# Kernel optimization log

Measured on AMD Instinct MI355X. Metric: run time of the kernel, lower is better.

## Reference

```python
import jax, jax.numpy as jnp
import numpy as np

D = 7            # tree max depth (n_locations = 4**D = 16384)
M = 128          # memory_dim
N_KEYS = sum(4 ** i for i in range(1, D + 1))      # 21844
N_INTERNAL = N_KEYS // 4                           # 5461


def setup_inputs() -> dict:
    key = jax.random.key(0)
    ks = jax.random.split(key, 6)
    B, C = 4096, 64
    hidden = jax.random.normal(ks[0], (B, C), dtype=jnp.float32)
    Wq = jax.random.normal(ks[1], (M, C), dtype=jnp.float32) * 0.05
    bq = jnp.zeros((M,), dtype=jnp.float32)
    states = jax.random.normal(ks[2], (N_KEYS, M), dtype=jnp.float32)
    Wk = jax.random.normal(ks[3], (D, M, M), dtype=jnp.float32) * 0.05
    bk = jnp.zeros((D, M), dtype=jnp.float32)
    return {"hidden": hidden, "Wq": Wq, "bq": bq, "states": states, "Wk": Wk, "bk": bk}


def reference(hidden, Wq, bq, states, Wk, bk):
    B = hidden.shape[0]
    # hidden_to_query (pre-training path uses class_to_query): [B, M]
    query = hidden @ Wq.T + bq
    # make_keys: per-depth state_to_key linear + activation on batch-independent states
    keys = []
    cursor = 0
    for i in range(D):
        n = 4 ** (i + 1)
        keys.append(jax.nn.relu(states[cursor:cursor + n] @ Wk[i].T + bk[i]))
        cursor += n
    keys = jnp.concatenate(keys, axis=0)               # [N_KEYS, M]
    # compute_scores: bmm(keys, query^T) -> [B, N_INTERNAL, 4]
    scores = jnp.einsum('km,bm->bk', keys, query).reshape(B, N_INTERNAL, 4)
    # to_location_distribution (is_consistent, pre_training): cumulative log-softmax down the tree
    logp = jax.nn.log_softmax(scores, axis=-1)         # [B, N_INTERNAL, 4]
    dists = []
    cur = None
    cursor = 0
    for d in range(1, D + 1):
        n_parents = 4 ** (d - 1)
        layer = logp[:, cursor:cursor + n_parents, :].reshape(B, 4 ** d)
        cur = layer if cur is None else jnp.repeat(cur, 4, axis=-1) + layer
        dists.append(cur)                              # [B, 4**d]
        cursor += n_parents
    return tuple(dists)
```

## Files before the change

### kernel.cpp

```cpp
#include <hip/hip_runtime.h>
#include <hip/hip_bf16.h>
#include <math.h>

#define MDIM 128
#define CDIM 64
#define NTILES 1366

typedef __attribute__((ext_vector_type(8))) __bf16 bf16x8;
typedef __attribute__((ext_vector_type(4))) float f32x4;

__global__ __launch_bounds__(256) void k_cvtw(const float* __restrict__ Wk,
                                              __hip_bfloat16* __restrict__ wkb) {
  const int i = blockIdx.x * 256 + threadIdx.x;
  float4 v = *reinterpret_cast<const float4*>(Wk + (size_t)i * 4);
  __hip_bfloat16 h[4];
  h[0] = __float2bfloat16(v.x); h[1] = __float2bfloat16(v.y);
  h[2] = __float2bfloat16(v.z); h[3] = __float2bfloat16(v.w);
  unsigned long long bits;
  __builtin_memcpy(&bits, h, 8);
  *reinterpret_cast<unsigned long long*>(wkb + (size_t)i * 4) = bits;
}

#define STR 144

__global__ __launch_bounds__(64) void k_keys_mfma(const float* __restrict__ states,
                                                  const __hip_bfloat16* __restrict__ wkb,
                                                  const float* __restrict__ bk,
                                                  bf16x8* __restrict__ keysF) {
  __shared__ __align__(16) __hip_bfloat16 sT[16 * STR];
  const int lane = threadIdx.x;
  const int c = lane & 15, hi = lane >> 4;
  int blk = blockIdx.x, d, t;
  if      (blk < 2)   { d = blk; t = 0; }
  else if (blk < 6)   { d = 2; t = blk - 2; }
  else if (blk < 22)  { d = 3; t = blk - 6; }
  else if (blk < 86)  { d = 4; t = blk - 22; }
  else if (blk < 342) { d = 5; t = blk - 86; }
  else                { d = 6; t = blk - 342; }
  const int cumArr[7] = {0, 4, 20, 84, 340, 1364, 5460};
  const int k0 = cumArr[d] + 16 * t;

  bf16x8 sb[4];
  const float* srow = states + (size_t)(k0 + c) * MDIM;
#pragma unroll
  for (int kf = 0; kf < 4; ++kf) {
    float4 a = *reinterpret_cast<const float4*>(srow + kf * 32 + hi * 8);
    float4 b = *reinterpret_cast<const float4*>(srow + kf * 32 + hi * 8 + 4);
    bf16x8 v;
    v[0] = (__bf16)a.x; v[1] = (__bf16)a.y; v[2] = (__bf16)a.z; v[3] = (__bf16)a.w;
    v[4] = (__bf16)b.x; v[5] = (__bf16)b.y; v[6] = (__bf16)b.z; v[7] = (__bf16)b.w;
    sb[kf] = v;
  }

  const __hip_bfloat16* wkd = wkb + (size_t)d * MDIM * MDIM;
  const float* bkd = bk + d * MDIM;

#pragma unroll
  for (int ct = 0; ct < 8; ++ct) {
    bf16x8 aw[4];
    const __hip_bfloat16* wrow = wkd + (size_t)(ct * 16 + c) * MDIM;
#pragma unroll
    for (int kf = 0; kf < 4; ++kf)
      aw[kf] = *reinterpret_cast<const bf16x8*>(wrow + kf * 32 + hi * 8);
    f32x4 acc = {};
#pragma unroll
    for (int kf = 0; kf < 4; ++kf)
      acc = __builtin_amdgcn_mfma_f32_16x16x32_bf16(aw[kf], sb[kf], acc, 0, 0, 0);
    float4 bias = *reinterpret_cast<const float4*>(bkd + ct * 16 + hi * 4);
    __hip_bfloat16 hv[4];
    hv[0] = __float2bfloat16(fmaxf(acc[0] + bias.x, 0.f));
    hv[1] = __float2bfloat16(fmaxf(acc[1] + bias.y, 0.f));
    hv[2] = __float2bfloat16(fmaxf(acc[2] + bias.z, 0.f));
    hv[3] = __float2bfloat16(fmaxf(acc[3] + bias.w, 0.f));
    unsigned long long bits;
    __builtin_memcpy(&bits, hv, 8);
    *reinterpret_cast<unsigned long long*>(&sT[c * STR + ct * 16 + 4 * hi]) = bits;
  }

#pragma unroll
  for (int kf = 0; kf < 4; ++kf) {
    bf16x8 v = *reinterpret_cast<const bf16x8*>(&sT[c * STR + kf * 32 + hi * 8]);
    keysF[(size_t)(blk * 4 + kf) * 64 + lane] = v;
  }
}

__global__ __launch_bounds__(128) void k_query(const float* __restrict__ hidden,
                                               const float* __restrict__ Wq,
                                               const float* __restrict__ bq,
                                               __hip_bfloat16* __restrict__ query) {
  __shared__ __align__(16) float sH[4][CDIM];
  const int b0 = blockIdx.x * 4;
  const int m  = threadIdx.x;
  for (int idx = m; idx < 4 * CDIM; idx += 128)
    sH[idx >> 6][idx & 63] = hidden[(size_t)b0 * CDIM + idx];
  __syncthreads();
  const float4* wrow = (const float4*)(Wq + (size_t)m * CDIM);
  float acc0 = 0.f, acc1 = 0.f, acc2 = 0.f, acc3 = 0.f;
#pragma unroll
  for (int kq = 0; kq < CDIM / 4; ++kq) {
    float4 w = wrow[kq];
    float4 a = *(const float4*)&sH[0][kq * 4];
    float4 b = *(const float4*)&sH[1][kq * 4];
    float4 c = *(const float4*)&sH[2][kq * 4];
    float4 e = *(const float4*)&sH[3][kq * 4];
    acc0 += w.x * a.x + w.y * a.y + w.z * a.z + w.w * a.w;
    acc1 += w.x * b.x + w.y * b.y + w.z * b.z + w.w * b.w;
    acc2 += w.x * c.x + w.y * c.y + w.z * c.z + w.w * c.w;
    acc3 += w.x * e.x + w.y * e.y + w.z * e.z + w.w * e.w;
  }
  const float bias = bq[m];
  query[(size_t)(b0 + 0) * MDIM + m] = __float2bfloat16(acc0 + bias);
  query[(size_t)(b0 + 1) * MDIM + m] = __float2bfloat16(acc1 + bias);
  query[(size_t)(b0 + 2) * MDIM + m] = __float2bfloat16(acc2 + bias);
  query[(size_t)(b0 + 3) * MDIM + m] = __float2bfloat16(acc3 + bias);
}

#define D7STR 68

struct Frag { bf16x8 f[4]; };

__device__ __forceinline__ void load_frags(const bf16x8* __restrict__ kF,
                                           int blk, Frag& fr, int lane) {
#pragma unroll
  for (int kf = 0; kf < 4; ++kf)
    fr.f[kf] = kF[(size_t)(blk * 4 + kf) * 64 + lane];
}

__device__ __forceinline__ float gather_par(const f32x4 cp, int u, int lane) {
  const int src = u * 16 + (lane & 15);
  const float g0 = __shfl(cp[0], src, 64);
  const float g1 = __shfl(cp[1], src, 64);
  const float g2 = __shfl(cp[2], src, 64);
  const float g3 = __shfl(cp[3], src, 64);
  const int hi = lane >> 4;
  const float p01 = (hi & 1) ? g1 : g0;
  const float p23 = (hi & 1) ? g3 : g2;
  return (hi & 2) ? p23 : p01;
}

__device__ __forceinline__ void tile_step(
    const bf16x8* __restrict__ kF, const Frag& cur, int nextBlk, Frag& nxt,
    const bf16x8 (&qf)[2][4], const f32x4* cumPrev, int u, f32x4 (&cumOut)[2],
    float* __restrict__ oPtr, size_t span, bool doStore, bool d1mask,
    float* __restrict__ ldsDst, int lane) {
  const int c = lane & 15, hi = lane >> 4;

  if (nextBlk >= 0) load_frags(kF, nextBlk, nxt, lane);

#pragma unroll
  for (int bt = 0; bt < 2; ++bt) {
    f32x4 acc = {};
    acc = __builtin_amdgcn_mfma_f32_16x16x32_bf16(cur.f[0], qf[bt][0], acc, 0, 0, 0);
    acc = __builtin_amdgcn_mfma_f32_16x16x32_bf16(cur.f[1], qf[bt][1], acc, 0, 0, 0);
    acc = __builtin_amdgcn_mfma_f32_16x16x32_bf16(cur.f[2], qf[bt][2], acc, 0, 0, 0);
    acc = __builtin_amdgcn_mfma_f32_16x16x32_bf16(cur.f[3], qf[bt][3], acc, 0, 0, 0);

    const float lse = __logf(__expf(acc[0]) + __expf(acc[1]) +
                             __expf(acc[2]) + __expf(acc[3]));
    float par = 0.f;
    if (cumPrev) par = gather_par(cumPrev[bt], u, lane);
    f32x4 cm;
    cm[0] = acc[0] - lse + par;
    cm[1] = acc[1] - lse + par;
    cm[2] = acc[2] - lse + par;
    cm[3] = acc[3] - lse + par;
    cumOut[bt] = cm;

    if (ldsDst) {
      *reinterpret_cast<f32x4*>(ldsDst + (bt * 16 + c) * D7STR) = cm;
    } else if (doStore && (!d1mask || hi == 0)) {
      float4 o;
      o.x = cm[0]; o.y = cm[1]; o.z = cm[2]; o.w = cm[3];
      *reinterpret_cast<float4*>(oPtr + (size_t)(bt * 16 + c) * span + hi * 4) = o;
    }
  }
}

__global__ __launch_bounds__(256) void k_tree(const bf16x8* __restrict__ kF,
                                              const __hip_bfloat16* __restrict__ query,
                                              float* __restrict__ out, int B) {
  __shared__ __align__(16) float sD7[4][32 * D7STR];
  __shared__ __align__(16) float sD6[4][32 * D7STR];

  const int tid  = threadIdx.x;
  const int lane = tid & 63;
  const int w    = tid >> 6;
  const int c    = lane & 15, hi = lane >> 4;

  const int S5  = blockIdx.x & 63;
  const int bg  = blockIdx.x >> 6;
  const int T4  = S5 >> 2;
  const int T3  = S5 >> 4;
  const int b0w = bg * 128 + w * 32;

  float* d7w = &sD7[w][0];
  float* d6w = &sD6[w][0];

  bf16x8 qf[2][4];
#pragma unroll
  for (int bt = 0; bt < 2; ++bt) {
    const __hip_bfloat16* qrow = query + (size_t)(b0w + bt * 16 + c) * MDIM;
#pragma unroll
    for (int kf = 0; kf < 4; ++kf)
      qf[bt][kf] = *reinterpret_cast<const bf16x8*>(qrow + kf * 32 + hi * 8);
  }

  Frag fA, fB;
  load_frags(kF, 0, fA, lane);

  f32x4 c1[2], c2[2], c3[2], c4[2], c5[2], c6[2], c7[2];

  tile_step(kF, fA, 1, fB, qf, nullptr, 0, c1,
            out + (size_t)b0w * 4, 4, S5 == 0, true, nullptr, lane);
  tile_step(kF, fB, 2 + T3, fA, qf, c1, 0, c2,
            out + (size_t)4 * B + (size_t)b0w * 16, 16, S5 == 0, false,
            nullptr, lane);
  tile_step(kF, fA, 6 + T4, fB, qf, c2, T3, c3,
            out + (size_t)20 * B + (size_t)b0w * 64 + 16 * T3, 64,
            (S5 & 15) == 0, false, nullptr, lane);
  tile_step(kF, fB, 22 + S5, fA, qf, c3, T4 & 3, c4,
            out + (size_t)84 * B + (size_t)b0w * 256 + 16 * T4, 256,
            (S5 & 3) == 0, false, nullptr, lane);
  tile_step(kF, fA, 86 + 4 * S5, fB, qf, c4, S5 & 3, c5,
            out + (size_t)340 * B + (size_t)b0w * 1024 + 16 * S5, 1024,
            true, false, nullptr, lane);

#pragma unroll
  for (int u5p = 0; u5p < 2; ++u5p) {
#pragma unroll
    for (int half = 0; half < 2; ++half) {
      const int u5 = u5p * 2 + half;
      Frag& f0 = (half == 0) ? fB : fA;
      Frag& f1 = (half == 0) ? fA : fB;
      const int T6 = 4 * S5 + u5;
      const int d7b = 342 + 16 * S5 + 4 * u5;
      tile_step(kF, f0, d7b, f1, qf, c5, u5, c6,
                nullptr, 0, false, false, d6w + u5 * 16 + hi * 4, lane);
      tile_step(kF, f1, d7b + 1, f0, qf, c6, 0, c7,
                nullptr, 0, false, false, d7w + 0 * 16 + hi * 4, lane);
      tile_step(kF, f0, d7b + 2, f1, qf, c6, 1, c7,
                nullptr, 0, false, false, d7w + 1 * 16 + hi * 4, lane);
      tile_step(kF, f1, d7b + 3, f0, qf, c6, 2, c7,
                nullptr, 0, false, false, d7w + 2 * 16 + hi * 4, lane);
      tile_step(kF, f0, (u5 < 3) ? (86 + 4 * S5 + u5 + 1) : -1, f1, qf, c6, 3, c7,
                nullptr, 0, false, false, d7w + 3 * 16 + hi * 4, lane);
      {
        float* dst = out + (size_t)5460 * B + (size_t)b0w * 16384 + 64 * T6;
#pragma unroll
        for (int j = 0; j < 8; ++j) {
          const int r = j * 4 + hi;
          f32x4 v = *reinterpret_cast<const f32x4*>(d7w + r * D7STR + c * 4);
          float4 o;
          o.x = v[0]; o.y = v[1]; o.z = v[2]; o.w = v[3];
          *reinterpret_cast<float4*>(dst + (size_t)r * 16384 + c * 4) = o;
        }
      }
    }
  }

  {
    float* dst = out + (size_t)1364 * B + (size_t)b0w * 4096 + 64 * S5;
#pragma unroll
    for (int j = 0; j < 8; ++j) {
      const int r = j * 4 + hi;
      f32x4 v = *reinterpret_cast<const f32x4*>(d6w + r * D7STR + c * 4);
      float4 o;
      o.x = v[0]; o.y = v[1]; o.z = v[2]; o.w = v[3];
      *reinterpret_cast<float4*>(dst + (size_t)r * 4096 + c * 4) = o;
    }
  }
}

extern "C" void kernel_launch(void* const* d_in, const int* in_sizes, int n_in,
                              void* d_out, int out_size, void* d_ws, size_t ws_size,
                              hipStream_t stream) {
  const float* hidden = (const float*)d_in[0];
  const float* Wq     = (const float*)d_in[1];
  const float* bq     = (const float*)d_in[2];
  const float* states = (const float*)d_in[3];
  const float* Wk     = (const float*)d_in[4];
  const float* bk     = (const float*)d_in[5];
  float* out = (float*)d_out;
  const int B = in_sizes[0] / CDIM;

  __hip_bfloat16* base  = (__hip_bfloat16*)d_ws;
  bf16x8* keysF = (bf16x8*)base;
  __hip_bfloat16* query = base + (size_t)NTILES * 4 * 64 * 8;
  __hip_bfloat16* wkb   = query + (size_t)B * MDIM;

  k_cvtw<<<(7 * MDIM * MDIM) / (256 * 4), 256, 0, stream>>>(Wk, wkb);
  k_query<<<B / 4, 128, 0, stream>>>(hidden, Wq, bq, query);
  k_keys_mfma<<<NTILES, 64, 0, stream>>>(states, wkb, bk, keysF);

  k_tree<<<(B / 128) * 64, 256, 0, stream>>>(keysF, query, out, B);
}
```

Baseline: 106.5 us.

## Remap tree blocks so waves share a batch tile; MFMA query projection

The tree kernel now gives each block 32 batch rows, with its four waves splitting the depth-5 subtrees (S5 = 4*chunk + w). Before, each block covered 128 rows at a single S5. Depth 1-4 tiles are computed redundantly per wave but stored only by wave 0, and depth-5 results are staged in shared memory so the block writes coalesced 64-wide row segments after a barrier. The query projection moves from scalar FMA to bf16 MFMA with an LDS transpose and vectorized stores. The remap changes redundant top-of-tree work and the output write pattern, and adds a block-wide sync plus extra LDS.

```diff
diff --git a/kernel.cpp b/kernel.cpp
--- a/kernel.cpp
+++ b/kernel.cpp
@@ -84,35 +84,56 @@
   }
 }
 
-__global__ __launch_bounds__(128) void k_query(const float* __restrict__ hidden,
-                                               const float* __restrict__ Wq,
-                                               const float* __restrict__ bq,
-                                               __hip_bfloat16* __restrict__ query) {
-  __shared__ __align__(16) float sH[4][CDIM];
-  const int b0 = blockIdx.x * 4;
-  const int m  = threadIdx.x;
-  for (int idx = m; idx < 4 * CDIM; idx += 128)
-    sH[idx >> 6][idx & 63] = hidden[(size_t)b0 * CDIM + idx];
-  __syncthreads();
-  const float4* wrow = (const float4*)(Wq + (size_t)m * CDIM);
-  float acc0 = 0.f, acc1 = 0.f, acc2 = 0.f, acc3 = 0.f;
-#pragma unroll
-  for (int kq = 0; kq < CDIM / 4; ++kq) {
-    float4 w = wrow[kq];
-    float4 a = *(const float4*)&sH[0][kq * 4];
-    float4 b = *(const float4*)&sH[1][kq * 4];
-    float4 c = *(const float4*)&sH[2][kq * 4];
-    float4 e = *(const float4*)&sH[3][kq * 4];
-    acc0 += w.x * a.x + w.y * a.y + w.z * a.z + w.w * a.w;
-    acc1 += w.x * b.x + w.y * b.y + w.z * b.z + w.w * b.w;
-    acc2 += w.x * c.x + w.y * c.y + w.z * c.z + w.w * c.w;
-    acc3 += w.x * e.x + w.y * e.y + w.z * e.z + w.w * e.w;
-  }
-  const float bias = bq[m];
-  query[(size_t)(b0 + 0) * MDIM + m] = __float2bfloat16(acc0 + bias);
-  query[(size_t)(b0 + 1) * MDIM + m] = __float2bfloat16(acc1 + bias);
-  query[(size_t)(b0 + 2) * MDIM + m] = __float2bfloat16(acc2 + bias);
-  query[(size_t)(b0 + 3) * MDIM + m] = __float2bfloat16(acc3 + bias);
+__global__ __launch_bounds__(64) void k_query_mfma(const float* __restrict__ hidden,
+                                                   const float* __restrict__ Wq,
+                                                   const float* __restrict__ bq,
+                                                   __hip_bfloat16* __restrict__ query) {
+  __shared__ __align__(16) __hip_bfloat16 sT[16 * STR];
+  const int lane = threadIdx.x;
+  const int c = lane & 15, hi = lane >> 4;
+  const int b0 = blockIdx.x * 16;
+
+  bf16x8 hb[2];
+  const float* hrow = hidden + (size_t)(b0 + c) * CDIM;
+#pragma unroll
+  for (int kf = 0; kf < 2; ++kf) {
+    float4 a = *reinterpret_cast<const float4*>(hrow + kf * 32 + hi * 8);
+    float4 b = *reinterpret_cast<const float4*>(hrow + kf * 32 + hi * 8 + 4);
+    bf16x8 v;
+    v[0] = (__bf16)a.x; v[1] = (__bf16)a.y; v[2] = (__bf16)a.z; v[3] = (__bf16)a.w;
+    v[4] = (__bf16)b.x; v[5] = (__bf16)b.y; v[6] = (__bf16)b.z; v[7] = (__bf16)b.w;
+    hb[kf] = v;
+  }
+
+#pragma unroll
+  for (int ct = 0; ct < 8; ++ct) {
+    const float* wrow = Wq + (size_t)(ct * 16 + c) * CDIM;
+    f32x4 acc = {};
+#pragma unroll
+    for (int kf = 0; kf < 2; ++kf) {
+      float4 a = *reinterpret_cast<const float4*>(wrow + kf * 32 + hi * 8);
+      float4 b = *reinterpret_cast<const float4*>(wrow + kf * 32 + hi * 8 + 4);
+      bf16x8 v;
+      v[0] = (__bf16)a.x; v[1] = (__bf16)a.y; v[2] = (__bf16)a.z; v[3] = (__bf16)a.w;
+      v[4] = (__bf16)b.x; v[5] = (__bf16)b.y; v[6] = (__bf16)b.z; v[7] = (__bf16)b.w;
+      acc = __builtin_amdgcn_mfma_f32_16x16x32_bf16(v, hb[kf], acc, 0, 0, 0);
+    }
+    float4 bias = *reinterpret_cast<const float4*>(bq + ct * 16 + hi * 4);
+    __hip_bfloat16 hv[4];
+    hv[0] = __float2bfloat16(acc[0] + bias.x);
+    hv[1] = __float2bfloat16(acc[1] + bias.y);
+    hv[2] = __float2bfloat16(acc[2] + bias.z);
+    hv[3] = __float2bfloat16(acc[3] + bias.w);
+    unsigned long long bits;
+    __builtin_memcpy(&bits, hv, 8);
+    *reinterpret_cast<unsigned long long*>(&sT[c * STR + ct * 16 + 4 * hi]) = bits;
+  }
+
+#pragma unroll
+  for (int kf = 0; kf < 4; ++kf) {
+    bf16x8 v = *reinterpret_cast<const bf16x8*>(&sT[c * STR + kf * 32 + hi * 8]);
+    *reinterpret_cast<bf16x8*>(query + (size_t)(b0 + c) * MDIM + kf * 32 + hi * 8) = v;
+  }
 }
 
 #define D7STR 68
@@ -181,17 +202,19 @@
                                               float* __restrict__ out, int B) {
   __shared__ __align__(16) float sD7[4][32 * D7STR];
   __shared__ __align__(16) float sD6[4][32 * D7STR];
+  __shared__ __align__(16) float sD5[32 * D7STR];
 
   const int tid  = threadIdx.x;
   const int lane = tid & 63;
   const int w    = tid >> 6;
   const int c    = lane & 15, hi = lane >> 4;
 
-  const int S5  = blockIdx.x & 63;
-  const int bg  = blockIdx.x >> 6;
-  const int T4  = S5 >> 2;
-  const int T3  = S5 >> 4;
-  const int b0w = bg * 128 + w * 32;
+  const int chunk = blockIdx.x & 15;
+  const int bg    = blockIdx.x >> 4;
+  const int S5    = 4 * chunk + w;
+  const int T4    = chunk;
+  const int T3    = chunk >> 2;
+  const int b0w   = bg * 32;
 
   float* d7w = &sD7[w][0];
   float* d6w = &sD6[w][0];
@@ -209,21 +232,21 @@
   load_frags(kF, 0, fA, lane);
 
   f32x4 c1[2], c2[2], c3[2], c4[2], c5[2], c6[2], c7[2];
+  const bool w0 = (w == 0);
 
   tile_step(kF, fA, 1, fB, qf, nullptr, 0, c1,
-            out + (size_t)b0w * 4, 4, S5 == 0, true, nullptr, lane);
+            out + (size_t)b0w * 4, 4, chunk == 0 && w0, true, nullptr, lane);
   tile_step(kF, fB, 2 + T3, fA, qf, c1, 0, c2,
-            out + (size_t)4 * B + (size_t)b0w * 16, 16, S5 == 0, false,
+            out + (size_t)4 * B + (size_t)b0w * 16, 16, chunk == 0 && w0, false,
             nullptr, lane);
   tile_step(kF, fA, 6 + T4, fB, qf, c2, T3, c3,
             out + (size_t)20 * B + (size_t)b0w * 64 + 16 * T3, 64,
-            (S5 & 15) == 0, false, nullptr, lane);
+            (chunk & 3) == 0 && w0, false, nullptr, lane);
   tile_step(kF, fB, 22 + S5, fA, qf, c3, T4 & 3, c4,
             out + (size_t)84 * B + (size_t)b0w * 256 + 16 * T4, 256,
-            (S5 & 3) == 0, false, nullptr, lane);
-  tile_step(kF, fA, 86 + 4 * S5, fB, qf, c4, S5 & 3, c5,
-            out + (size_t)340 * B + (size_t)b0w * 1024 + 16 * S5, 1024,
-            true, false, nullptr, lane);
+            w0, false, nullptr, lane);
+  tile_step(kF, fA, 86 + 4 * S5, fB, qf, c4, w, c5,
+            nullptr, 0, false, false, &sD5[0] + w * 16 + hi * 4, lane);
 
 #pragma unroll
   for (int u5p = 0; u5p < 2; ++u5p) {
@@ -269,6 +292,20 @@
       *reinterpret_cast<float4*>(dst + (size_t)r * 4096 + c * 4) = o;
     }
   }
+
+  __syncthreads();
+  {
+    float* dst = out + (size_t)340 * B + (size_t)b0w * 1024 + 64 * chunk;
+    const int r16 = tid >> 4, c16 = tid & 15;
+#pragma unroll
+    for (int j = 0; j < 2; ++j) {
+      const int r = j * 16 + r16;
+      f32x4 v = *reinterpret_cast<const f32x4*>(&sD5[0] + r * D7STR + c16 * 4);
+      float4 o;
+      o.x = v[0]; o.y = v[1]; o.z = v[2]; o.w = v[3];
+      *reinterpret_cast<float4*>(dst + (size_t)r * 1024 + c16 * 4) = o;
+    }
+  }
 }
 
 extern "C" void kernel_launch(void* const* d_in, const int* in_sizes, int n_in,
@@ -289,8 +326,8 @@
   __hip_bfloat16* wkb   = query + (size_t)B * MDIM;
 
   k_cvtw<<<(7 * MDIM * MDIM) / (256 * 4), 256, 0, stream>>>(Wk, wkb);
-  k_query<<<B / 4, 128, 0, stream>>>(hidden, Wq, bq, query);
+  k_query_mfma<<<B / 16, 64, 0, stream>>>(hidden, Wq, bq, query);
   k_keys_mfma<<<NTILES, 64, 0, stream>>>(states, wkb, bk, keysF);
 
-  k_tree<<<(B / 128) * 64, 256, 0, stream>>>(keysF, query, out, B);
-}
+  k_tree<<<(B / 32) * 16, 256, 0, stream>>>(keysF, query, out, B);
+}
```

Measured after the change: 107.2 us. About the same (+0.7%).

## Fuse weight conversion, query projection and key MFMA into one prep kernel

Applied to the files above, without the earlier changes.

Removes the separate Wk bf16 conversion and scalar query kernels. A single launch now computes keys with MFMA while converting fp32 Wk to bf16 inline, and computes the query projection on extra blocks with bf16 MFMA. This cuts two kernel launches and the intermediate wkb buffer, at the cost of redundant per-block fp32 weight loads and conversions. It also lowers the query projection's precision to bf16 inputs.

```diff
diff --git a/kernel.cpp b/kernel.cpp
--- a/kernel.cpp
+++ b/kernel.cpp
@@ -9,28 +9,63 @@
 typedef __attribute__((ext_vector_type(8))) __bf16 bf16x8;
 typedef __attribute__((ext_vector_type(4))) float f32x4;
 
-__global__ __launch_bounds__(256) void k_cvtw(const float* __restrict__ Wk,
-                                              __hip_bfloat16* __restrict__ wkb) {
-  const int i = blockIdx.x * 256 + threadIdx.x;
-  float4 v = *reinterpret_cast<const float4*>(Wk + (size_t)i * 4);
-  __hip_bfloat16 h[4];
-  h[0] = __float2bfloat16(v.x); h[1] = __float2bfloat16(v.y);
-  h[2] = __float2bfloat16(v.z); h[3] = __float2bfloat16(v.w);
-  unsigned long long bits;
-  __builtin_memcpy(&bits, h, 8);
-  *reinterpret_cast<unsigned long long*>(wkb + (size_t)i * 4) = bits;
-}
-
 #define STR 144
 
-__global__ __launch_bounds__(64) void k_keys_mfma(const float* __restrict__ states,
-                                                  const __hip_bfloat16* __restrict__ wkb,
-                                                  const float* __restrict__ bk,
-                                                  bf16x8* __restrict__ keysF) {
+__device__ __forceinline__ bf16x8 cvt8(const float* p, int off) {
+  float4 a = *reinterpret_cast<const float4*>(p + off);
+  float4 b = *reinterpret_cast<const float4*>(p + off + 4);
+  bf16x8 v;
+  v[0] = (__bf16)a.x; v[1] = (__bf16)a.y; v[2] = (__bf16)a.z; v[3] = (__bf16)a.w;
+  v[4] = (__bf16)b.x; v[5] = (__bf16)b.y; v[6] = (__bf16)b.z; v[7] = (__bf16)b.w;
+  return v;
+}
+
+__global__ __launch_bounds__(64) void k_prep(const float* __restrict__ states,
+                                             const float* __restrict__ Wk,
+                                             const float* __restrict__ bk,
+                                             const float* __restrict__ hidden,
+                                             const float* __restrict__ Wq,
+                                             const float* __restrict__ bq,
+                                             bf16x8* __restrict__ keysF,
+                                             __hip_bfloat16* __restrict__ query) {
   __shared__ __align__(16) __hip_bfloat16 sT[16 * STR];
   const int lane = threadIdx.x;
   const int c = lane & 15, hi = lane >> 4;
-  int blk = blockIdx.x, d, t;
+  int blk = blockIdx.x;
+
+  if (blk >= NTILES) {
+    const int b0 = (blk - NTILES) * 16;
+    bf16x8 hb[2];
+    const float* hrow = hidden + (size_t)(b0 + c) * CDIM;
+#pragma unroll
+    for (int kf = 0; kf < 2; ++kf) hb[kf] = cvt8(hrow, kf * 32 + hi * 8);
+#pragma unroll
+    for (int ct = 0; ct < 8; ++ct) {
+      const float* wrow = Wq + (size_t)(ct * 16 + c) * CDIM;
+      f32x4 acc = {};
+#pragma unroll
+      for (int kf = 0; kf < 2; ++kf)
+        acc = __builtin_amdgcn_mfma_f32_16x16x32_bf16(cvt8(wrow, kf * 32 + hi * 8),
+                                                      hb[kf], acc, 0, 0, 0);
+      float4 bias = *reinterpret_cast<const float4*>(bq + ct * 16 + hi * 4);
+      __hip_bfloat16 hv[4];
+      hv[0] = __float2bfloat16(acc[0] + bias.x);
+      hv[1] = __float2bfloat16(acc[1] + bias.y);
+      hv[2] = __float2bfloat16(acc[2] + bias.z);
+      hv[3] = __float2bfloat16(acc[3] + bias.w);
+      unsigned long long bits;
+      __builtin_memcpy(&bits, hv, 8);
+      *reinterpret_cast<unsigned long long*>(&sT[c * STR + ct * 16 + 4 * hi]) = bits;
+    }
+#pragma unroll
+    for (int kf = 0; kf < 4; ++kf) {
+      bf16x8 v = *reinterpret_cast<const bf16x8*>(&sT[c * STR + kf * 32 + hi * 8]);
+      *reinterpret_cast<bf16x8*>(query + (size_t)(b0 + c) * MDIM + kf * 32 + hi * 8) = v;
+    }
+    return;
+  }
+
+  int d, t;
   if      (blk < 2)   { d = blk; t = 0; }
   else if (blk < 6)   { d = 2; t = blk - 2; }
   else if (blk < 22)  { d = 3; t = blk - 6; }
@@ -43,29 +78,19 @@
   bf16x8 sb[4];
   const float* srow = states + (size_t)(k0 + c) * MDIM;
 #pragma unroll
-  for (int kf = 0; kf < 4; ++kf) {
-    float4 a = *reinterpret_cast<const float4*>(srow + kf * 32 + hi * 8);
-    float4 b = *reinterpret_cast<const float4*>(srow + kf * 32 + hi * 8 + 4);
-    bf16x8 v;
-    v[0] = (__bf16)a.x; v[1] = (__bf16)a.y; v[2] = (__bf16)a.z; v[3] = (__bf16)a.w;
-    v[4] = (__bf16)b.x; v[5] = (__bf16)b.y; v[6] = (__bf16)b.z; v[7] = (__bf16)b.w;
-    sb[kf] = v;
-  }
-
-  const __hip_bfloat16* wkd = wkb + (size_t)d * MDIM * MDIM;
+  for (int kf = 0; kf < 4; ++kf) sb[kf] = cvt8(srow, kf * 32 + hi * 8);
+
+  const float* wkd = Wk + (size_t)d * MDIM * MDIM;
   const float* bkd = bk + d * MDIM;
 
 #pragma unroll
   for (int ct = 0; ct < 8; ++ct) {
-    bf16x8 aw[4];
-    const __hip_bfloat16* wrow = wkd + (size_t)(ct * 16 + c) * MDIM;
+    const float* wrow = wkd + (size_t)(ct * 16 + c) * MDIM;
+    f32x4 acc = {};
 #pragma unroll
     for (int kf = 0; kf < 4; ++kf)
-      aw[kf] = *reinterpret_cast<const bf16x8*>(wrow + kf * 32 + hi * 8);
-    f32x4 acc = {};
-#pragma unroll
-    for (int kf = 0; kf < 4; ++kf)
-      acc = __builtin_amdgcn_mfma_f32_16x16x32_bf16(aw[kf], sb[kf], acc, 0, 0, 0);
+      acc = __builtin_amdgcn_mfma_f32_16x16x32_bf16(cvt8(wrow, kf * 32 + hi * 8),
+                                                    sb[kf], acc, 0, 0, 0);
     float4 bias = *reinterpret_cast<const float4*>(bkd + ct * 16 + hi * 4);
     __hip_bfloat16 hv[4];
     hv[0] = __float2bfloat16(fmaxf(acc[0] + bias.x, 0.f));
@@ -82,37 +107,6 @@
     bf16x8 v = *reinterpret_cast<const bf16x8*>(&sT[c * STR + kf * 32 + hi * 8]);
     keysF[(size_t)(blk * 4 + kf) * 64 + lane] = v;
   }
-}
-
-__global__ __launch_bounds__(128) void k_query(const float* __restrict__ hidden,
-                                               const float* __restrict__ Wq,
-                                               const float* __restrict__ bq,
-                                               __hip_bfloat16* __restrict__ query) {
-  __shared__ __align__(16) float sH[4][CDIM];
-  const int b0 = blockIdx.x * 4;
-  const int m  = threadIdx.x;
-  for (int idx = m; idx < 4 * CDIM; idx += 128)
-    sH[idx >> 6][idx & 63] = hidden[(size_t)b0 * CDIM + idx];
-  __syncthreads();
-  const float4* wrow = (const float4*)(Wq + (size_t)m * CDIM);
-  float acc0 = 0.f, acc1 = 0.f, acc2 = 0.f, acc3 = 0.f;
-#pragma unroll
-  for (int kq = 0; kq < CDIM / 4; ++kq) {
-    float4 w = wrow[kq];
-    float4 a = *(const float4*)&sH[0][kq * 4];
-    float4 b = *(const float4*)&sH[1][kq * 4];
-    float4 c = *(const float4*)&sH[2][kq * 4];
-    float4 e = *(const float4*)&sH[3][kq * 4];
-    acc0 += w.x * a.x + w.y * a.y + w.z * a.z + w.w * a.w;
-    acc1 += w.x * b.x + w.y * b.y + w.z * b.z + w.w * b.w;
-    acc2 += w.x * c.x + w.y * c.y + w.z * c.z + w.w * c.w;
-    acc3 += w.x * e.x + w.y * e.y + w.z * e.z + w.w * e.w;
-  }
-  const float bias = bq[m];
-  query[(size_t)(b0 + 0) * MDIM + m] = __float2bfloat16(acc0 + bias);
-  query[(size_t)(b0 + 1) * MDIM + m] = __float2bfloat16(acc1 + bias);
-  query[(size_t)(b0 + 2) * MDIM + m] = __float2bfloat16(acc2 + bias);
-  query[(size_t)(b0 + 3) * MDIM + m] = __float2bfloat16(acc3 + bias);
 }
 
 #define D7STR 68
@@ -286,11 +280,9 @@
   __hip_bfloat16* base  = (__hip_bfloat16*)d_ws;
   bf16x8* keysF = (bf16x8*)base;
   __hip_bfloat16* query = base + (size_t)NTILES * 4 * 64 * 8;
-  __hip_bfloat16* wkb   = query + (size_t)B * MDIM;
-
-  k_cvtw<<<(7 * MDIM * MDIM) / (256 * 4), 256, 0, stream>>>(Wk, wkb);
-  k_query<<<B / 4, 128, 0, stream>>>(hidden, Wq, bq, query);
-  k_keys_mfma<<<NTILES, 64, 0, stream>>>(states, wkb, bk, keysF);
+
+  k_prep<<<NTILES + B / 16, 64, 0, stream>>>(states, Wk, bk, hidden, Wq, bq,
+                                             keysF, query);
 
   k_tree<<<(B / 128) * 64, 256, 0, stream>>>(keysF, query, out, B);
 }
```

New measurement: 100.8 us. -5.3%, faster.
